# Performance work log

Measured on AMD Instinct MI355X. Metric: run time of the kernel, lower is better.

The kernel has to match this reference:

```python
import jax, jax.numpy as jnp
import numpy as np

N_NODES = 200000
N_EDGES = 3200000
N_FEAT = 128
N_GRAPHS = 1000
N_CLASSES = 10
K = 30          # sort-pool k
C_CAT = 97      # 32+32+32+1 concatenated channels


def _glorot(k, shape):
    fan = shape[0] + shape[-1]
    return jax.random.normal(k, shape, jnp.float32) * (2.0 / fan) ** 0.5


def setup_inputs() -> dict:
    key = jax.random.key(0)
    ks = jax.random.split(key, 20)
    x = jax.random.normal(ks[0], (N_NODES, N_FEAT), jnp.float32)
    edge_index = jax.random.randint(ks[1], (2, N_EDGES), 0, N_NODES, jnp.int32)
    batch = jnp.sort(jax.random.randint(ks[2], (N_NODES,), 0, N_GRAPHS, jnp.int32))
    params = dict(
        W1=_glorot(ks[3], (N_FEAT, 32)), b1=jnp.zeros((32,), jnp.float32),
        W2=_glorot(ks[4], (32, 32)),     b2=jnp.zeros((32,), jnp.float32),
        W3=_glorot(ks[5], (32, 32)),     b3=jnp.zeros((32,), jnp.float32),
        W4=_glorot(ks[6], (32, 1)),      b4=jnp.zeros((1,), jnp.float32),
        conv5_w=_glorot(ks[7], (16, 1, 97)),  conv5_b=jnp.zeros((16,), jnp.float32),
        conv6_w=_glorot(ks[8], (32, 16, 5)),  conv6_b=jnp.zeros((32,), jnp.float32),
        fc1_w=_glorot(ks[9], (352, 128)),     fc1_b=jnp.zeros((128,), jnp.float32),
        fc2_w=_glorot(ks[10], (128, N_CLASSES)), fc2_b=jnp.zeros((N_CLASSES,), jnp.float32),
    )
    return dict(x=x, edge_index=edge_index, batch=batch, **params)


def reference(x, edge_index, batch, W1, b1, W2, b2, W3, b3, W4, b4,
              conv5_w, conv5_b, conv6_w, conv6_b, fc1_w, fc1_b, fc2_w, fc2_b):
    N = x.shape[0]
    src, dst = edge_index[0], edge_index[1]
    emask = (src != dst).astype(x.dtype)            # remove_self_loops
    deg = jax.ops.segment_sum(emask, dst, num_segments=N) + 1.0  # +1 for added self-loop
    inv_sqrt = jax.lax.rsqrt(deg)
    coef = emask * inv_sqrt[src] * inv_sqrt[dst]    # D^-1/2 (A) D^-1/2 edge weight
    inv_deg = 1.0 / deg                             # self-loop weight

    def gcn(h, W, b):
        hw = h @ W
        agg = jax.ops.segment_sum(hw[src] * coef[:, None], dst, num_segments=N)
        return agg + hw * inv_deg[:, None] + b

    x1 = jnp.tanh(gcn(x, W1, b1))
    x2 = jnp.tanh(gcn(x1, W2, b2))
    x3 = jnp.tanh(gcn(x2, W3, b3))
    x4 = jnp.tanh(gcn(x3, W4, b4))
    xc = jnp.concatenate([x1, x2, x3, x4], axis=-1)  # [N, 97]

    # SortAggregation(k=30): per-graph descending sort by last channel, top-k, zero pad
    perm = jnp.lexsort((-xc[:, -1], batch))          # batch-major, last channel desc
    xs, bs = xc[perm], batch[perm]
    counts = jax.ops.segment_sum(jnp.ones_like(batch), batch, num_segments=N_GRAPHS)
    starts = jnp.cumsum(counts) - counts
    rank = jnp.arange(N, dtype=jnp.int32) - starts[bs]
    valid = rank < K
    pooled = jnp.zeros((N_GRAPHS, K, C_CAT), xc.dtype).at[
        bs, jnp.where(valid, rank, K - 1)].add(jnp.where(valid[:, None], xs, 0.0))

    z = pooled.reshape(N_GRAPHS, 1, K * C_CAT)       # [G, 1, 2910]
    dn = ('NCH', 'OIH', 'NCH')
    z = jax.lax.conv_general_dilated(z, conv5_w, (97,), 'VALID', dimension_numbers=dn)
    z = jax.nn.relu(z + conv5_b[None, :, None])      # [G, 16, 30]
    z = jax.lax.reduce_window(z, -jnp.inf, jax.lax.max, (1, 1, 2), (1, 1, 2), 'VALID')
    z = jax.lax.conv_general_dilated(z, conv6_w, (1,), 'VALID', dimension_numbers=dn)
    z = jax.nn.relu(z + conv6_b[None, :, None])      # [G, 32, 11]
    z = z.reshape(N_GRAPHS, -1)                      # [G, 352]
    h = jax.nn.relu(z @ fc1_w + fc1_b)               # dropout is identity in eval
    return jax.nn.log_softmax(h @ fc2_w + fc2_b, axis=-1)
```

## Files before the change

kernel.cpp:

```cpp
#include <hip/hip_runtime.h>
#include <math.h>

#define NN 200000
#define NE 3200000
#define NF 128
#define NG 1000
#define KSEL 30
#define CCAT 97
#define NPAD 200704
#define SCAN_BLKS 196
#define EPADCAP (NE + 8 * NN)

#define BWID 512
#define NB 391
#define BCAP 10240
#define P1_CHUNK 8192
#define P1_BLKS 391

__global__ void k_p1_partition(const int* __restrict__ ei, int* __restrict__ bcursor,
                               int* __restrict__ ebuf) {
    __shared__ int lhist[NB];
    __shared__ int lbase[NB];
    int tid = threadIdx.x;
    int base = blockIdx.x * P1_CHUNK;
    for (int b = tid; b < NB; b += 256) lhist[b] = 0;
    __syncthreads();
    for (int it = 0; it < P1_CHUNK / 256; it++) {
        int e = base + it * 256 + tid;
        if (e < NE) {
            int s = ei[e], d = ei[NE + e];
            if (s != d) atomicAdd(&lhist[d >> 9], 1);
        }
    }
    __syncthreads();
    for (int b = tid; b < NB; b += 256) {
        int cnt = lhist[b];
        lbase[b] = cnt ? atomicAdd(&bcursor[b], cnt) : 0;
        lhist[b] = 0;
    }
    __syncthreads();
    for (int it = 0; it < P1_CHUNK / 256; it++) {
        int e = base + it * 256 + tid;
        if (e < NE) {
            int s = ei[e], d = ei[NE + e];
            if (s != d) {
                int b = d >> 9;
                int r = atomicAdd(&lhist[b], 1);
                int pos = lbase[b] + r;
                if (pos >= BCAP) pos = BCAP - 1;
                ebuf[b * BCAP + pos] = s | ((d & 511) << 18);
            }
        }
    }
}

__global__ void k_p2_count(const int* __restrict__ bcursor, const int* __restrict__ ebuf,
                           int* __restrict__ rowcnt, float* __restrict__ inv_sqrt) {
    __shared__ int lcnt[BWID];
    int b = blockIdx.x;
    int tid = threadIdx.x;
    for (int i = tid; i < BWID; i += 256) lcnt[i] = 0;
    __syncthreads();
    int size = bcursor[b];
    if (size > BCAP) size = BCAP;
    const int* eb = ebuf + b * BCAP;
    for (int k = tid; k < size; k += 256) atomicAdd(&lcnt[eb[k] >> 18], 1);
    __syncthreads();
    int node0 = b * BWID;
    for (int i = tid; i < BWID; i += 256) {
        int node = node0 + i;
        if (node < NN) {
            int c = lcnt[i];
            rowcnt[node] = (c + 7) & ~7;
            inv_sqrt[node] = rsqrtf((float)(c + 1));
        }
    }
}

__global__ void k_scanA(const int* __restrict__ in, int* __restrict__ out,
                        int* __restrict__ bsums) {
    __shared__ int s[1024];
    int tid = threadIdx.x;
    int gid = blockIdx.x * 1024 + tid;
    int v = in[gid];
    s[tid] = v;
    __syncthreads();
    for (int off = 1; off < 1024; off <<= 1) {
        int a = (tid >= off) ? s[tid - off] : 0;
        int cur = s[tid];
        __syncthreads();
        s[tid] = cur + a;
        __syncthreads();
    }
    out[gid] = s[tid] - v;
    if (tid == 1023) bsums[blockIdx.x] = s[tid];
}

__global__ void k_scanB(int* __restrict__ bsums) {
    __shared__ int s[256];
    int tid = threadIdx.x;
    int v = (tid < SCAN_BLKS) ? bsums[tid] : 0;
    s[tid] = v;
    __syncthreads();
    for (int off = 1; off < 256; off <<= 1) {
        int a = (tid >= off) ? s[tid - off] : 0;
        int cur = s[tid];
        __syncthreads();
        s[tid] = cur + a;
        __syncthreads();
    }
    if (tid < SCAN_BLKS) bsums[tid] = s[tid] - v;
}

__global__ void k_scanC(int* __restrict__ out, const int* __restrict__ bsums) {
    int gid = blockIdx.x * 1024 + threadIdx.x;
    out[gid] += bsums[blockIdx.x];
}

__global__ void k_p3_scatter(const int* __restrict__ bcursor, const int* __restrict__ ebuf,
                             const int* __restrict__ rowstart, int* __restrict__ esrc) {
    __shared__ int lcur[BWID];
    int b = blockIdx.x;
    int tid = threadIdx.x;
    int node0 = b * BWID;
    for (int i = tid; i < BWID; i += 256) lcur[i] = rowstart[node0 + i];
    __syncthreads();
    int size = bcursor[b];
    if (size > BCAP) size = BCAP;
    const int* eb = ebuf + b * BCAP;
    for (int k = tid; k < size; k += 256) {
        int v = eb[k];
        int local = v >> 18;
        int pos = atomicAdd(&lcur[local], 1);
        esrc[pos] = v & 0x3FFFF;
    }
    __syncthreads();
    for (int i = tid; i < BWID; i += 256) {
        int node = node0 + i;
        if (node < NN) {
            int end = rowstart[node + 1];
            for (int p = lcur[i]; p < end; p++) esrc[p] = NN;
        }
    }
}

template <int K>
__global__ void __launch_bounds__(256, 3) k_mm(const float* __restrict__ X,
                                               const float* __restrict__ W,
                                               const float* __restrict__ inv_sqrt,
                                               float* __restrict__ Y) {
    constexpr int K4 = K / 4;
    constexpr int RS = K4 + 1;
    __shared__ float4 sW[K * 8];
    __shared__ float4 sX[64 * RS];
    int tid = threadIdx.x;
    for (int i = tid; i < K * 8; i += 256) sW[i] = ((const float4*)W)[i];
    const float4* __restrict__ Xg = (const float4*)(X + (size_t)blockIdx.x * 64 * K);
    for (int i = tid; i < 64 * K4; i += 256) {
        int row = i / K4;
        int col = i & (K4 - 1);
        sX[row * RS + col] = Xg[i];
    }
    __syncthreads();
    int g = tid >> 3;
    int q = tid & 7;
    int r0 = blockIdx.x * 64 + g * 2;
    const float4* __restrict__ xr0 = &sX[(size_t)(g * 2 + 0) * RS];
    const float4* __restrict__ xr1 = &sX[(size_t)(g * 2 + 1) * RS];
    float4 a0 = make_float4(0.f, 0.f, 0.f, 0.f);
    float4 a1 = make_float4(0.f, 0.f, 0.f, 0.f);
#pragma unroll 4
    for (int k4 = 0; k4 < K4; k4++) {
        float4 x0 = xr0[k4];
        float4 x1 = xr1[k4];
        const float4* wk = &sW[k4 * 32 + q];
#pragma unroll
        for (int kk = 0; kk < 4; kk++) {
            float4 w = wk[kk * 8];
            float s0 = (kk == 0) ? x0.x : (kk == 1) ? x0.y : (kk == 2) ? x0.z : x0.w;
            float s1 = (kk == 0) ? x1.x : (kk == 1) ? x1.y : (kk == 2) ? x1.z : x1.w;
            a0.x = fmaf(s0, w.x, a0.x); a0.y = fmaf(s0, w.y, a0.y);
            a0.z = fmaf(s0, w.z, a0.z); a0.w = fmaf(s0, w.w, a0.w);
            a1.x = fmaf(s1, w.x, a1.x); a1.y = fmaf(s1, w.y, a1.y);
            a1.z = fmaf(s1, w.z, a1.z); a1.w = fmaf(s1, w.w, a1.w);
        }
    }
    float s0 = inv_sqrt[r0 + 0];
    float s1 = inv_sqrt[r0 + 1];
    a0.x *= s0; a0.y *= s0; a0.z *= s0; a0.w *= s0;
    a1.x *= s1; a1.y *= s1; a1.z *= s1; a1.w *= s1;
    ((float4*)(Y + (size_t)(r0 + 0) * 32))[q] = a0;
    ((float4*)(Y + (size_t)(r0 + 1) * 32))[q] = a1;
}

template <int MODE>
__global__ void k_aggr_f(const int* __restrict__ rowstart, const int* __restrict__ esrc,
                         const float* __restrict__ hws, const float* __restrict__ inv_sqrt,
                         const float* __restrict__ bvec, const float* __restrict__ Wn,
                         float* __restrict__ xout, float* __restrict__ hnext) {
    __shared__ float sxr[8][32];
    int t = blockIdx.x * 256 + threadIdx.x;
    int n = t >> 5, c = t & 31;
    int e0 = rowstart[n], e1 = rowstart[n + 1];
    float a[8];
    a[0] = hws[(size_t)n * 32 + c];
#pragma unroll
    for (int k = 1; k < 8; k++) a[k] = 0.0f;
    for (int e = e0; e < e1; e += 8) {
        int4 sA = *(const int4*)(esrc + e);
        int4 sB = *(const int4*)(esrc + e + 4);
        float v0 = hws[(size_t)sA.x * 32 + c];
        float v1 = hws[(size_t)sA.y * 32 + c];
        float v2 = hws[(size_t)sA.z * 32 + c];
        float v3 = hws[(size_t)sA.w * 32 + c];
        float v4 = hws[(size_t)sB.x * 32 + c];
        float v5 = hws[(size_t)sB.y * 32 + c];
        float v6 = hws[(size_t)sB.z * 32 + c];
        float v7 = hws[(size_t)sB.w * 32 + c];
        a[0] += v0; a[1] += v1; a[2] += v2; a[3] += v3;
        a[4] += v4; a[5] += v5; a[6] += v6; a[7] += v7;
    }
    float acc = ((a[0] + a[1]) + (a[2] + a[3])) + ((a[4] + a[5]) + (a[6] + a[7]));
    float invs = inv_sqrt[n];
    float r = tanhf(fmaf(acc, invs, bvec[c]));
    xout[t] = r;
    if (MODE == 1) {
        int ln = threadIdx.x >> 5;
        sxr[ln][c] = r;
        float wcol[32];
#pragma unroll
        for (int k = 0; k < 32; k++) wcol[k] = Wn[k * 32 + c];
        __syncthreads();
        const float4* xr = (const float4*)sxr[ln];
        float h = 0.f;
#pragma unroll
        for (int j = 0; j < 8; j++) {
            float4 xq = xr[j];
            h = fmaf(xq.x, wcol[4 * j + 0], h);
            h = fmaf(xq.y, wcol[4 * j + 1], h);
            h = fmaf(xq.z, wcol[4 * j + 2], h);
            h = fmaf(xq.w, wcol[4 * j + 3], h);
        }
        hnext[t] = h * invs;
    } else {
        float v = r * Wn[c];
        v += __shfl_xor(v, 1);
        v += __shfl_xor(v, 2);
        v += __shfl_xor(v, 4);
        v += __shfl_xor(v, 8);
        v += __shfl_xor(v, 16);
        if (c == 0) hnext[n] = v * invs;
        if (t == 0) hnext[NN] = 0.f;
    }
}

__global__ void k_aggr1(const int* __restrict__ rowstart, const int* __restrict__ esrc,
                        const float* __restrict__ hws4, const float* __restrict__ inv_sqrt,
                        const float* __restrict__ b4, float* __restrict__ x4) {
    int n = blockIdx.x * 256 + threadIdx.x;
    if (n >= NN) return;
    int e0 = rowstart[n], e1 = rowstart[n + 1];
    float a[8];
    a[0] = hws4[n];
#pragma unroll
    for (int k = 1; k < 8; k++) a[k] = 0.0f;
    for (int e = e0; e < e1; e += 8) {
        int4 sA = *(const int4*)(esrc + e);
        int4 sB = *(const int4*)(esrc + e + 4);
        a[0] += hws4[sA.x]; a[1] += hws4[sA.y];
        a[2] += hws4[sA.z]; a[3] += hws4[sA.w];
        a[4] += hws4[sB.x]; a[5] += hws4[sB.y];
        a[6] += hws4[sB.z]; a[7] += hws4[sB.w];
    }
    float acc = ((a[0] + a[1]) + (a[2] + a[3])) + ((a[4] + a[5]) + (a[6] + a[7]));
    x4[n] = tanhf(fmaf(acc, inv_sqrt[n], b4[0]));
}

__global__ void k_gbounds(const int* __restrict__ batch, int* __restrict__ starts) {
    int n = blockIdx.x * 256 + threadIdx.x;
    if (n >= NN) return;
    int bn = batch[n];
    int bp = (n == 0) ? -1 : batch[n - 1];
    for (int g = bp + 1; g <= bn; g++) starts[g] = n;
    if (n == NN - 1)
        for (int g = bn + 1; g <= NG; g++) starts[g] = NN;
}

__global__ void k_tail(const int* __restrict__ starts,
                       const float* __restrict__ x1, const float* __restrict__ x2,
                       const float* __restrict__ x3, const float* __restrict__ x4,
                       const float* __restrict__ w5, const float* __restrict__ b5,
                       const float* __restrict__ w6, const float* __restrict__ b6,
                       const float* __restrict__ fw1, const float* __restrict__ fb1,
                       const float* __restrict__ fw2, const float* __restrict__ fb2,
                       float* __restrict__ out) {
    __shared__ float keys[1024];
    __shared__ int sel[KSEL];
    __shared__ float sP[KSEL * CCAT];
    __shared__ float s5[16 * 30];
    __shared__ float smp[16 * 15];
    __shared__ float sz[352];
    __shared__ float sh[128];
    __shared__ float sl[10];
    int g = blockIdx.x;
    int tid = threadIdx.x;
    int start = starts[g];
    int cnt = starts[g + 1] - start;
    if (cnt > 1024) cnt = 1024;
    for (int i = tid; i < cnt; i += 256) keys[i] = x4[start + i];
    __syncthreads();
    for (int i = tid; i < cnt; i += 256) {
        float ki = keys[i];
        int rank = 0;
        for (int j = 0; j < cnt; j++) {
            float kj = keys[j];
            rank += (kj > ki) || (kj == ki && j < i);
        }
        if (rank < KSEL) sel[rank] = start + i;
    }
    __syncthreads();
    int selcnt = cnt < KSEL ? cnt : KSEL;
    for (int t = tid; t < KSEL * CCAT; t += 256) {
        int r = t / CCAT, ch = t - r * CCAT;
        float v = 0.0f;
        if (r < selcnt) {
            int node = sel[r];
            if (ch < 32)      v = x1[(size_t)node * 32 + ch];
            else if (ch < 64) v = x2[(size_t)node * 32 + ch - 32];
            else if (ch < 96) v = x3[(size_t)node * 32 + ch - 64];
            else              v = x4[node];
        }
        sP[t] = v;
    }
    __syncthreads();
    for (int t = tid; t < 16 * 30; t += 256) {
        int c = t / 30, j = t - c * 30;
        float acc = b5[c];
        for (int i = 0; i < CCAT; i++) acc = fmaf(sP[j * CCAT + i], w5[c * CCAT + i], acc);
        s5[c * 30 + j] = fmaxf(acc, 0.0f);
    }
    __syncthreads();
    for (int t = tid; t < 16 * 15; t += 256) {
        int c = t / 15, j = t - c * 15;
        smp[t] = fmaxf(s5[c * 30 + 2 * j], s5[c * 30 + 2 * j + 1]);
    }
    __syncthreads();
    for (int t = tid; t < 32 * 11; t += 256) {
        int c = t / 11, j = t - c * 11;
        float acc = b6[c];
        for (int ci = 0; ci < 16; ci++) {
#pragma unroll
            for (int k = 0; k < 5; k++)
                acc = fmaf(smp[ci * 15 + j + k], w6[(c * 16 + ci) * 5 + k], acc);
        }
        sz[t] = fmaxf(acc, 0.0f);
    }
    __syncthreads();
    if (tid < 128) {
        float acc = fb1[tid];
        for (int i = 0; i < 352; i++) acc = fmaf(sz[i], fw1[i * 128 + tid], acc);
        sh[tid] = fmaxf(acc, 0.0f);
    }
    __syncthreads();
    if (tid < 10) {
        float acc = fb2[tid];
        for (int i = 0; i < 128; i++) acc = fmaf(sh[i], fw2[i * 10 + tid], acc);
        sl[tid] = acc;
    }
    __syncthreads();
    if (tid < 10) {
        float m = -1e30f;
        for (int i = 0; i < 10; i++) m = fmaxf(m, sl[i]);
        float ssum = 0.0f;
        for (int i = 0; i < 10; i++) ssum += expf(sl[i] - m);
        out[g * 10 + tid] = sl[tid] - m - logf(ssum);
    }
}

extern "C" void kernel_launch(void* const* d_in, const int* in_sizes, int n_in,
                              void* d_out, int out_size, void* d_ws, size_t ws_size,
                              hipStream_t stream) {
    const float* x   = (const float*)d_in[0];
    const int*   ei  = (const int*)d_in[1];
    const int*   bat = (const int*)d_in[2];
    const float* W1  = (const float*)d_in[3];
    const float* b1  = (const float*)d_in[4];
    const float* W2  = (const float*)d_in[5];
    const float* b2  = (const float*)d_in[6];
    const float* W3  = (const float*)d_in[7];
    const float* b3  = (const float*)d_in[8];
    const float* W4  = (const float*)d_in[9];
    const float* b4  = (const float*)d_in[10];
    const float* w5  = (const float*)d_in[11];
    const float* b5  = (const float*)d_in[12];
    const float* w6  = (const float*)d_in[13];
    const float* b6  = (const float*)d_in[14];
    const float* fw1 = (const float*)d_in[15];
    const float* fb1 = (const float*)d_in[16];
    const float* fw2 = (const float*)d_in[17];
    const float* fb2 = (const float*)d_in[18];
    float* out = (float*)d_out;

    float* ws = (float*)d_ws;
    float* inv_sqrt = ws;
    float* hwsA     = inv_sqrt + NN;
    float* hwsB     = hwsA + (size_t)(NN + 1) * 32;
    float* x1       = hwsB + (size_t)(NN + 1) * 32;
    float* x2       = x1 + (size_t)NN * 32;
    float* x3       = x2 + (size_t)NN * 32;
    float* x4       = x3 + (size_t)NN * 32;
    int* rowcnt     = (int*)(x4 + NN);
    int* rowstart   = rowcnt + NPAD;
    int* esrc       = rowstart + NPAD;
    int* bcursor    = esrc + EPADCAP;
    int* bsums      = bcursor + 512;
    int* gstarts    = bsums + 256;
    int* ebuf       = (int*)x3;

    const int TB = 256;
    int gN  = (NN + TB - 1) / TB;
    int gNC = (NN * 32) / TB;
    int gMM = NN / 64;

    hipMemsetAsync(bcursor, 0, 512 * sizeof(int), stream);
    hipMemsetAsync(rowcnt, 0, NPAD * sizeof(int), stream);
    hipMemsetAsync(hwsA + (size_t)NN * 32, 0, 32 * sizeof(float), stream);
    hipMemsetAsync(hwsB + (size_t)NN * 32, 0, 32 * sizeof(float), stream);
    k_p1_partition<<<P1_BLKS, TB, 0, stream>>>(ei, bcursor, ebuf);
    k_p2_count<<<NB, TB, 0, stream>>>(bcursor, ebuf, rowcnt, inv_sqrt);
    k_scanA<<<SCAN_BLKS, 1024, 0, stream>>>(rowcnt, rowstart, bsums);
    k_scanB<<<1, 256, 0, stream>>>(bsums);
    k_scanC<<<SCAN_BLKS, 1024, 0, stream>>>(rowstart, bsums);
    k_p3_scatter<<<NB, TB, 0, stream>>>(bcursor, ebuf, rowstart, esrc);

    k_gbounds<<<gN, TB, 0, stream>>>(bat, gstarts);

    k_mm<128><<<gMM, TB, 0, stream>>>(x, W1, inv_sqrt, hwsA);
    k_aggr_f<1><<<gNC, TB, 0, stream>>>(rowstart, esrc, hwsA, inv_sqrt, b1, W2, x1, hwsB);
    k_aggr_f<1><<<gNC, TB, 0, stream>>>(rowstart, esrc, hwsB, inv_sqrt, b2, W3, x2, hwsA);
    k_aggr_f<2><<<gNC, TB, 0, stream>>>(rowstart, esrc, hwsA, inv_sqrt, b3, W4, x3, hwsB);
    k_aggr1<<<gN, TB, 0, stream>>>(rowstart, esrc, hwsB, inv_sqrt, b4, x4);

    k_tail<<<NG, TB, 0, stream>>>(gstarts, x1, x2, x3, x4,
                                  w5, b5, w6, b6, fw1, fb1, fw2, fb2, out);
}
```

Baseline: 575.1 us.

## Replace global prefix scan with per-bucket atomic offset allocation in CSR build

```diff
diff --git a/kernel.cpp b/kernel.cpp
--- a/kernel.cpp
+++ b/kernel.cpp
@@ -7,8 +7,6 @@
 #define NG 1000
 #define KSEL 30
 #define CCAT 97
-#define NPAD 200704
-#define SCAN_BLKS 196
 #define EPADCAP (NE + 8 * NN)
 
 #define BWID 512
@@ -16,6 +14,7 @@
 #define BCAP 10240
 #define P1_CHUNK 8192
 #define P1_BLKS 391
+#define GCUR 400
 
 __global__ void k_p1_partition(const int* __restrict__ ei, int* __restrict__ bcursor,
                                int* __restrict__ ebuf) {
@@ -55,10 +54,18 @@
 }
 
 __global__ void k_p2_count(const int* __restrict__ bcursor, const int* __restrict__ ebuf,
-                           int* __restrict__ rowcnt, float* __restrict__ inv_sqrt) {
+                           int* __restrict__ rowstart, int* __restrict__ rowcnt8,
+                           float* __restrict__ inv_sqrt, int* __restrict__ gcursor,
+                           float* __restrict__ hwsA, float* __restrict__ hwsB) {
     __shared__ int lcnt[BWID];
+    __shared__ int ps[256];
+    __shared__ int sbase;
     int b = blockIdx.x;
     int tid = threadIdx.x;
+    if (b == 0 && tid < 32) {
+        hwsA[(size_t)NN * 32 + tid] = 0.0f;
+        hwsB[(size_t)NN * 32 + tid] = 0.0f;
+    }
     for (int i = tid; i < BWID; i += 256) lcnt[i] = 0;
     __syncthreads();
     int size = bcursor[b];
@@ -67,63 +74,47 @@
     for (int k = tid; k < size; k += 256) atomicAdd(&lcnt[eb[k] >> 18], 1);
     __syncthreads();
     int node0 = b * BWID;
-    for (int i = tid; i < BWID; i += 256) {
-        int node = node0 + i;
-        if (node < NN) {
-            int c = lcnt[i];
-            rowcnt[node] = (c + 7) & ~7;
-            inv_sqrt[node] = rsqrtf((float)(c + 1));
-        }
-    }
-}
-
-__global__ void k_scanA(const int* __restrict__ in, int* __restrict__ out,
-                        int* __restrict__ bsums) {
-    __shared__ int s[1024];
-    int tid = threadIdx.x;
-    int gid = blockIdx.x * 1024 + tid;
-    int v = in[gid];
-    s[tid] = v;
-    __syncthreads();
-    for (int off = 1; off < 1024; off <<= 1) {
-        int a = (tid >= off) ? s[tid - off] : 0;
-        int cur = s[tid];
+    int i0 = 2 * tid, i1 = 2 * tid + 1;
+    int c0raw = lcnt[i0], c1raw = lcnt[i1];
+    int c0 = (node0 + i0 < NN) ? ((c0raw + 7) & ~7) : 0;
+    int c1 = (node0 + i1 < NN) ? ((c1raw + 7) & ~7) : 0;
+    int pair = c0 + c1;
+    ps[tid] = pair;
+    __syncthreads();
+    for (int off = 1; off < 256; off <<= 1) {
+        int a = (tid >= off) ? ps[tid - off] : 0;
+        int cur = ps[tid];
         __syncthreads();
-        s[tid] = cur + a;
+        ps[tid] = cur + a;
         __syncthreads();
     }
-    out[gid] = s[tid] - v;
-    if (tid == 1023) bsums[blockIdx.x] = s[tid];
-}
-
-__global__ void k_scanB(int* __restrict__ bsums) {
-    __shared__ int s[256];
-    int tid = threadIdx.x;
-    int v = (tid < SCAN_BLKS) ? bsums[tid] : 0;
-    s[tid] = v;
-    __syncthreads();
-    for (int off = 1; off < 256; off <<= 1) {
-        int a = (tid >= off) ? s[tid - off] : 0;
-        int cur = s[tid];
-        __syncthreads();
-        s[tid] = cur + a;
-        __syncthreads();
-    }
-    if (tid < SCAN_BLKS) bsums[tid] = s[tid] - v;
-}
-
-__global__ void k_scanC(int* __restrict__ out, const int* __restrict__ bsums) {
-    int gid = blockIdx.x * 1024 + threadIdx.x;
-    out[gid] += bsums[blockIdx.x];
+    if (tid == 255) sbase = atomicAdd(gcursor, ps[255]);
+    int excl = ps[tid] - pair;
+    __syncthreads();
+    int rs0 = sbase + excl;
+    int rs1 = rs0 + c0;
+    int n0 = node0 + i0, n1 = node0 + i1;
+    if (n0 < NN) {
+        rowstart[n0] = rs0;
+        rowcnt8[n0] = c0;
+        inv_sqrt[n0] = rsqrtf((float)(c0raw + 1));
+    }
+    if (n1 < NN) {
+        rowstart[n1] = rs1;
+        rowcnt8[n1] = c1;
+        inv_sqrt[n1] = rsqrtf((float)(c1raw + 1));
+    }
 }
 
 __global__ void k_p3_scatter(const int* __restrict__ bcursor, const int* __restrict__ ebuf,
-                             const int* __restrict__ rowstart, int* __restrict__ esrc) {
+                             const int* __restrict__ rowstart, const int* __restrict__ rowcnt8,
+                             int* __restrict__ esrc) {
     __shared__ int lcur[BWID];
     int b = blockIdx.x;
     int tid = threadIdx.x;
     int node0 = b * BWID;
-    for (int i = tid; i < BWID; i += 256) lcur[i] = rowstart[node0 + i];
+    for (int i = tid; i < BWID; i += 256)
+        lcur[i] = (node0 + i < NN) ? rowstart[node0 + i] : 0;
     __syncthreads();
     int size = bcursor[b];
     if (size > BCAP) size = BCAP;
@@ -138,7 +129,7 @@
     for (int i = tid; i < BWID; i += 256) {
         int node = node0 + i;
         if (node < NN) {
-            int end = rowstart[node + 1];
+            int end = rowstart[node] + rowcnt8[node];
             for (int p = lcur[i]; p < end; p++) esrc[p] = NN;
         }
     }
@@ -194,14 +185,15 @@
 }
 
 template <int MODE>
-__global__ void k_aggr_f(const int* __restrict__ rowstart, const int* __restrict__ esrc,
+__global__ void k_aggr_f(const int* __restrict__ rowstart, const int* __restrict__ rowcnt8,
+                         const int* __restrict__ esrc,
                          const float* __restrict__ hws, const float* __restrict__ inv_sqrt,
                          const float* __restrict__ bvec, const float* __restrict__ Wn,
                          float* __restrict__ xout, float* __restrict__ hnext) {
     __shared__ float sxr[8][32];
     int t = blockIdx.x * 256 + threadIdx.x;
     int n = t >> 5, c = t & 31;
-    int e0 = rowstart[n], e1 = rowstart[n + 1];
+    int e0 = rowstart[n], e1 = e0 + rowcnt8[n];
     float a[8];
     a[0] = hws[(size_t)n * 32 + c];
 #pragma unroll
@@ -254,12 +246,13 @@
     }
 }
 
-__global__ void k_aggr1(const int* __restrict__ rowstart, const int* __restrict__ esrc,
+__global__ void k_aggr1(const int* __restrict__ rowstart, const int* __restrict__ rowcnt8,
+                        const int* __restrict__ esrc,
                         const float* __restrict__ hws4, const float* __restrict__ inv_sqrt,
                         const float* __restrict__ b4, float* __restrict__ x4) {
     int n = blockIdx.x * 256 + threadIdx.x;
     if (n >= NN) return;
-    int e0 = rowstart[n], e1 = rowstart[n + 1];
+    int e0 = rowstart[n], e1 = e0 + rowcnt8[n];
     float a[8];
     a[0] = hws4[n];
 #pragma unroll
@@ -409,12 +402,11 @@
     float* x2       = x1 + (size_t)NN * 32;
     float* x3       = x2 + (size_t)NN * 32;
     float* x4       = x3 + (size_t)NN * 32;
-    int* rowcnt     = (int*)(x4 + NN);
-    int* rowstart   = rowcnt + NPAD;
-    int* esrc       = rowstart + NPAD;
+    int* rowstart   = (int*)(x4 + NN);
+    int* rowcnt8    = rowstart + NN;
+    int* esrc       = rowcnt8 + NN;
     int* bcursor    = esrc + EPADCAP;
-    int* bsums      = bcursor + 512;
-    int* gstarts    = bsums + 256;
+    int* gstarts    = bcursor + 512;
     int* ebuf       = (int*)x3;
 
     const int TB = 256;
@@ -423,23 +415,18 @@
     int gMM = NN / 64;
 
     hipMemsetAsync(bcursor, 0, 512 * sizeof(int), stream);
-    hipMemsetAsync(rowcnt, 0, NPAD * sizeof(int), stream);
-    hipMemsetAsync(hwsA + (size_t)NN * 32, 0, 32 * sizeof(float), stream);
-    hipMemsetAsync(hwsB + (size_t)NN * 32, 0, 32 * sizeof(float), stream);
     k_p1_partition<<<P1_BLKS, TB, 0, stream>>>(ei, bcursor, ebuf);
-    k_p2_count<<<NB, TB, 0, stream>>>(bcursor, ebuf, rowcnt, inv_sqrt);
-    k_scanA<<<SCAN_BLKS, 1024, 0, stream>>>(rowcnt, rowstart, bsums);
-    k_scanB<<<1, 256, 0, stream>>>(bsums);
-    k_scanC<<<SCAN_BLKS, 1024, 0, stream>>>(rowstart, bsums);
-    k_p3_scatter<<<NB, TB, 0, stream>>>(bcursor, ebuf, rowstart, esrc);
+    k_p2_count<<<NB, TB, 0, stream>>>(bcursor, ebuf, rowstart, rowcnt8, inv_sqrt,
+                                      bcursor + GCUR, hwsA, hwsB);
+    k_p3_scatter<<<NB, TB, 0, stream>>>(bcursor, ebuf, rowstart, rowcnt8, esrc);
 
     k_gbounds<<<gN, TB, 0, stream>>>(bat, gstarts);
 
     k_mm<128><<<gMM, TB, 0, stream>>>(x, W1, inv_sqrt, hwsA);
-    k_aggr_f<1><<<gNC, TB, 0, stream>>>(rowstart, esrc, hwsA, inv_sqrt, b1, W2, x1, hwsB);
-    k_aggr_f<1><<<gNC, TB, 0, stream>>>(rowstart, esrc, hwsB, inv_sqrt, b2, W3, x2, hwsA);
-    k_aggr_f<2><<<gNC, TB, 0, stream>>>(rowstart, esrc, hwsA, inv_sqrt, b3, W4, x3, hwsB);
-    k_aggr1<<<gN, TB, 0, stream>>>(rowstart, esrc, hwsB, inv_sqrt, b4, x4);
+    k_aggr_f<1><<<gNC, TB, 0, stream>>>(rowstart, rowcnt8, esrc, hwsA, inv_sqrt, b1, W2, x1, hwsB);
+    k_aggr_f<1><<<gNC, TB, 0, stream>>>(rowstart, rowcnt8, esrc, hwsB, inv_sqrt, b2, W3, x2, hwsA);
+    k_aggr_f<2><<<gNC, TB, 0, stream>>>(rowstart, rowcnt8, esrc, hwsA, inv_sqrt, b3, W4, x3, hwsB);
+    k_aggr1<<<gN, TB, 0, stream>>>(rowstart, rowcnt8, esrc, hwsB, inv_sqrt, b4, x4);
 
     k_tail<<<NG, TB, 0, stream>>>(gstarts, x1, x2, x3, x4,
                                   w5, b5, w6, b6, fw1, fb1, fw2, fb2, out);
```

Result: no change. 570.2 us (-0.9%).
